# Performance work log

Measured on AMD Instinct MI355X. Metric: run time of the kernel, lower is better.

The kernel has to match this reference:

```python
import jax, jax.numpy as jnp
import numpy as np
from jax import lax

B, C, H, W = 1, 128, 56, 56
NH, NG, KS = 4, 1, 3
CG = C // NG          # channels per group
CH = C // NH          # channels per head
NHG = NH // NG        # heads per group
SCALE = CH ** -0.5


def _norm_grid(h, w, n):
    # matches _get_normalized_grid: (y, x) order, each normalized to [-1, 1]
    y = jnp.arange(h, dtype=jnp.float32) / (h - 1.0) * 2.0 - 1.0
    x = jnp.arange(w, dtype=jnp.float32) / (w - 1.0) * 2.0 - 1.0
    g = jnp.stack(jnp.meshgrid(y, x, indexing='ij'), axis=-1)  # (h, w, 2)
    return jnp.broadcast_to(g[None], (n, h, w, 2))


def _grid_sample(img, grid):
    # F.grid_sample: bilinear, align_corners=True, zeros padding; grid is (x, y) in [-1, 1]
    n, c, hi, wi = img.shape
    gs = grid.shape[1:-1]
    gx = grid[..., 0].reshape(n, -1)
    gy = grid[..., 1].reshape(n, -1)
    fx = (gx + 1.0) * 0.5 * (wi - 1)
    fy = (gy + 1.0) * 0.5 * (hi - 1)
    x0 = jnp.floor(fx)
    y0 = jnp.floor(fy)
    wx = fx - x0
    wy = fy - y0
    x0 = x0.astype(jnp.int32)
    y0 = y0.astype(jnp.int32)
    imgf = img.reshape(n, c, hi * wi)

    def corner(xi, yi, wgt):
        valid = (xi >= 0) & (xi < wi) & (yi >= 0) & (yi < hi)
        idx = jnp.clip(yi, 0, hi - 1) * wi + jnp.clip(xi, 0, wi - 1)
        vals = jax.vmap(lambda im, ii: jnp.take(im, ii, axis=1))(imgf, idx)  # (n, c, P)
        return vals * (wgt * valid)[:, None, :]

    out = (corner(x0, y0, (1 - wx) * (1 - wy)) + corner(x0 + 1, y0, wx * (1 - wy))
           + corner(x0, y0 + 1, (1 - wx) * wy) + corner(x0 + 1, y0 + 1, wx * wy))
    return out.reshape((n, c) + gs)


def _conv1x1(t, w, b):
    return jnp.einsum('bchw,oc->bohw', t, w) + b[None, :, None, None]


def _forward(x, query, dw_w, dw_b, ln_w, ln_b, pw_w, k_w, k_b, v_w, v_b, out_w, out_b, rpe_table):
    # conv_offset: depthwise 3x3 (stride 1, pad 1) -> channel LayerNorm -> GELU -> 1x1 to 2ch (no bias)
    qg = query.reshape(B * NG, CG, H, W)
    t = lax.conv_general_dilated(qg, dw_w, (1, 1), ((1, 1), (1, 1)),
                                 dimension_numbers=('NCHW', 'OIHW', 'NCHW'),
                                 feature_group_count=CG) + dw_b[None, :, None, None]
    mu = t.mean(axis=1, keepdims=True)
    var = ((t - mu) ** 2).mean(axis=1, keepdims=True)
    t = (t - mu) / jnp.sqrt(var + 1e-5) * ln_w[None, :, None, None] + ln_b[None, :, None, None]
    t = jax.nn.gelu(t, approximate=False)
    offset = jnp.einsum('bchw,oc->bohw', t, pw_w)  # (BG, 2, Hk, Wk) in (y, x) order
    Hk, Wk = offset.shape[-2:]
    n_sample = Hk * Wk

    # tanh-scaled offsets (scale_offset_range=True, factor 0.5)
    rng = jnp.array([1.0 / (Hk - 1.0), 1.0 / (Wk - 1.0)], jnp.float32).reshape(1, 2, 1, 1)
    offset = jnp.tanh(offset) * rng * 0.5
    offset = jnp.transpose(offset, (0, 2, 3, 1))  # (BG, Hk, Wk, 2)

    ref = _norm_grid(Hk, Wk, B * NG)
    rwo = offset + ref  # no clamp in the scale_offset_range branch

    # sample K/V features at deformed locations
    xs = _grid_sample(x.reshape(B * NG, CG, H, W), rwo[..., ::-1])  # (BG, CG, Hk, Wk)
    xs = xs.reshape(B, C, 1, n_sample)

    q = query.reshape(B * NH, CH, H * W)
    k = _conv1x1(xs, k_w, k_b).reshape(B * NH, CH, n_sample)
    v = _conv1x1(xs, v_w, v_b).reshape(B * NH, CH, n_sample)

    attn = jnp.einsum('bcm,bcn->bmn', q, k) * SCALE  # (B*NH, HW, n_sample)

    # relative position bias via bilinear lookup of rpe_table at displacements
    rpe = jnp.broadcast_to(rpe_table[None], (B,) + rpe_table.shape).reshape(B * NG, NHG, 2 * H - 1, 2 * W - 1)
    qgrid = _norm_grid(H, W, B * NG)
    disp = (qgrid.reshape(B * NG, H * W, 2)[:, :, None, :]
            - rwo.reshape(B * NG, n_sample, 2)[:, None, :, :]) * 0.5  # (BG, HW, n_sample, 2)
    bias = _grid_sample(rpe, disp[..., ::-1]).reshape(B * NH, H * W, n_sample)

    attn = jax.nn.softmax(attn + bias, axis=2)
    out = jnp.einsum('bmn,bcn->bcm', attn, v).reshape(B, C, H, W)
    return _conv1x1(out, out_w, out_b)


def setup_inputs() -> dict:
    key = jax.random.key(0)
    ks = jax.random.split(key, 8)
    f = lambda k, sh, s=0.02: jax.random.normal(k, sh, jnp.float32) * s
    return {
        'x': jax.random.normal(ks[0], (B, C, H, W), jnp.float32),
        'query': jax.random.normal(ks[1], (B, C, H, W), jnp.float32),
        'dw_w': f(ks[2], (CG, 1, KS, KS)),
        'dw_b': jnp.zeros((CG,), jnp.float32),
        'ln_w': jnp.ones((CG,), jnp.float32),
        'ln_b': jnp.zeros((CG,), jnp.float32),
        'pw_w': f(ks[3], (2, CG)),
        'k_w': f(ks[4], (C, C)),
        'k_b': jnp.zeros((C,), jnp.float32),
        'v_w': f(ks[5], (C, C)),
        'v_b': jnp.zeros((C,), jnp.float32),
        'out_w': f(ks[6], (C, C)),
        'out_b': jnp.zeros((C,), jnp.float32),
        'rpe_table': f(ks[7], (NH, 2 * H - 1, 2 * W - 1), 0.01),
    }


def reference(x, query, dw_w, dw_b, ln_w, ln_b, pw_w, k_w, k_b, v_w, v_b, out_w, out_b, rpe_table):
    return _forward(x, query, dw_w, dw_b, ln_w, ln_b, pw_w, k_w, k_b, v_w, v_b, out_w, out_b, rpe_table)
```

## Files before the change

kernel.cpp:

```cpp
#include <hip/hip_runtime.h>
#include <hip/hip_bf16.h>
#include <math.h>

#define HH 56
#define WW 56
#define HW 3136
#define NHEAD 4
#define RP 111
#define TP 113
#define TPE 12769
#define SCALE 0.17677669529663687f
#define LOG2E 1.44269504088896f
#define QSC (SCALE * LOG2E)
#define CLEN 224
#define BLEN 448
#define NSTEP 7

typedef unsigned short ushortT;
typedef __attribute__((ext_vector_type(8))) short short8v;
typedef __attribute__((ext_vector_type(16))) float f32x16;

#define OFF_AA   8192u
#define OFF_W4   12288u
#define OFF_KBF  24832u
#define OFF_VBF  225536u
#define OFF_QBF  426240u
#define OFF_KWT  1028352u
#define OFF_VWT  1044736u
#define OFF_OWT  1061120u
#define OFF_XT   1077504u
#define OFF_QT   1478912u
#define OFF_TP2  1880320u
#define OFF_ATT2 1982976u
#define OFF_SUM  (OFF_ATT2 + 401408u)
#define ZERO_F4  103504u

__device__ __forceinline__ ushortT f2bf(float f) {
    unsigned u = __float_as_uint(f);
    u += 0x7fffu + ((u >> 16) & 1u);
    return (ushortT)(u >> 16);
}

__device__ __forceinline__ unsigned cvtpk(float lo, float hi) {
    unsigned r;
    asm("v_cvt_pk_bf16_f32 %0, %1, %2" : "=v"(r) : "v"(lo), "v"(hi));
    return r;
}

__device__ __forceinline__ float fexp2(float x) {
    float r;
    asm("v_exp_f32 %0, %1" : "=v"(r) : "v"(x));
    return r;
}

__device__ __forceinline__ float wave_sum(float v) {
#pragma unroll
    for (int o = 1; o < 64; o <<= 1) v += __shfl_xor(v, o);
    return v;
}

__global__ __launch_bounds__(256) void prep_all_kernel(
    const float* __restrict__ kw, const float* __restrict__ vw, const float* __restrict__ ow,
    const float* __restrict__ rpe, const float* __restrict__ x, const float* __restrict__ query,
    float* __restrict__ kwT, float* __restrict__ vwT, float* __restrict__ owT,
    float2* __restrict__ tp2, float* __restrict__ xT, float* __restrict__ qT,
    ushortT* __restrict__ qbf, float* __restrict__ zbase) {
    const int job = blockIdx.y;
    __shared__ float tile[32][33];
    if (job < 3) {
        int i = blockIdx.x * 256 + threadIdx.x;
        if (i >= 16384) return;
        const float* srcw = (job == 0) ? kw : (job == 1) ? vw : ow;
        float* dstw       = (job == 0) ? kwT : (job == 1) ? vwT : owT;
        dstw[(i & 127) * 128 + (i >> 7)] = srcw[i];
    } else if (job == 3) {
        int i = blockIdx.x * 256 + threadIdx.x;
        if (i >= NHEAD * TPE) return;
        int hd = i / TPE, r = i % TPE;
        int py = r / TP, px = r % TP;
        float v0 = 0.f, v1 = 0.f;
        if (py >= 1 && py <= RP) {
            if (px >= 1 && px <= RP) v0 = rpe[hd * RP * RP + (py - 1) * RP + (px - 1)] * LOG2E;
            if (px <= RP - 1)        v1 = rpe[hd * RP * RP + (py - 1) * RP + px] * LOG2E;
        }
        tp2[i] = make_float2(v0, v1);
    } else if (job == 6) {
        int i = blockIdx.x * 256 + threadIdx.x;
        if (i < ZERO_F4) ((float4*)zbase)[i] = make_float4(0.f, 0.f, 0.f, 0.f);
    } else {
        int bx = blockIdx.x;
        if (bx >= 392) return;
        const float* src = (job == 5) ? query : x;
        float* dst       = (job == 5) ? qT : xT;
        int pt = (bx % 98) * 32, ct = (bx / 98) * 32;
        int jj = threadIdx.x & 31, ii = threadIdx.x >> 5;
#pragma unroll
        for (int r = 0; r < 4; r++)
            tile[ii + r * 8][jj] = src[(ct + ii + r * 8) * HW + pt + jj];
        __syncthreads();
#pragma unroll
        for (int r = 0; r < 4; r++) {
            int p = pt + ii + r * 8, cc = ct + jj;
            float val = tile[jj][ii + r * 8];
            dst[p * 128 + cc] = val;
            if (job == 5)
                qbf[(size_t)((cc >> 5) * HW + p) * 32 + (cc & 31)] = f2bf(val * QSC);
        }
    }
}

__global__ __launch_bounds__(128) void sample_kv_kernel(
    const float* __restrict__ xT, const float* __restrict__ qT,
    const float* __restrict__ dww, const float* __restrict__ dwb,
    const float* __restrict__ lnw, const float* __restrict__ lnb,
    const float* __restrict__ pww,
    const float* __restrict__ kwT, const float* __restrict__ vwT,
    const float* __restrict__ kb, const float* __restrict__ vb,
    ushortT* __restrict__ kbf, ushortT* __restrict__ vbf,
    int* __restrict__ aa, float4* __restrict__ w4g) {
    const int n0 = blockIdx.x * 8;
    const int tid = threadIdx.x;
    const int h = n0 / WW, w0 = n0 % WW;
    const int wid = tid >> 6;
    const bool l0 = ((tid & 63) == 0);

    __shared__ float xs[128 * 9];
    __shared__ int   cidx[8][4];
    __shared__ float cw[8][4];
    __shared__ ushortT kst[8][128];
    __shared__ float red_a[2][8], red_b[2][8], red_y[2][8], red_x[2][8];

    float dwwr[9];
#pragma unroll
    for (int k = 0; k < 9; k++) dwwr[k] = dww[tid * 9 + k];
    float qv[3][10];
#pragma unroll
    for (int ky = 0; ky < 3; ky++) {
        int yy = h + ky - 1;
        bool vy = (unsigned)yy < (unsigned)HH;
#pragma unroll
        for (int t = 0; t < 10; t++) {
            int xx = w0 + t - 1;
            bool v = vy && ((unsigned)xx < (unsigned)WW);
            qv[ky][t] = v ? qT[(yy * WW + xx) * 128 + tid] : 0.f;
        }
    }
    float tj[8];
#pragma unroll
    for (int j = 0; j < 8; j++) {
        float t = dwb[tid];
#pragma unroll
        for (int ky = 0; ky < 3; ky++)
#pragma unroll
            for (int kx = 0; kx < 3; kx++)
                t += qv[ky][j + kx] * dwwr[ky * 3 + kx];
        tj[j] = t;
    }
#pragma unroll
    for (int j = 0; j < 8; j++) { float s = wave_sum(tj[j]); if (l0) red_a[wid][j] = s; }
    __syncthreads();
    float dj[8];
#pragma unroll
    for (int j = 0; j < 8; j++) {
        float mu = (red_a[0][j] + red_a[1][j]) * (1.f / 128.f);
        dj[j] = tj[j] - mu;
        float s = wave_sum(dj[j] * dj[j]);
        if (l0) red_b[wid][j] = s;
    }
    __syncthreads();
    float py = pww[tid], px = pww[128 + tid];
#pragma unroll
    for (int j = 0; j < 8; j++) {
        float var = (red_b[0][j] + red_b[1][j]) * (1.f / 128.f);
        float tn = dj[j] / sqrtf(var + 1e-5f) * lnw[tid] + lnb[tid];
        float g = 0.5f * tn * (1.f + erff(tn * 0.70710678118654752f));
        float sy = wave_sum(g * py);
        float sx = wave_sum(g * px);
        if (l0) { red_y[wid][j] = sy; red_x[wid][j] = sx; }
    }
    __syncthreads();

    if (tid < 8) {
        int j = tid;
        float thy = tanhf(red_y[0][j] + red_y[1][j]);
        float thx = tanhf(red_x[0][j] + red_x[1][j]);
        int hh = h, ww2 = w0 + j;
        float gy = thy * (0.5f / 55.f) + ((float)hh * (2.f / 55.f) - 1.f);
        float gx = thx * (0.5f / 55.f) + ((float)ww2 * (2.f / 55.f) - 1.f);
        float fx = (gx + 1.f) * 27.5f;
        float fy = (gy + 1.f) * 27.5f;
        float x0f = floorf(fx), y0f = floorf(fy);
        float wx = fx - x0f, wy = fy - y0f;
        int x0 = (int)x0f, y0 = (int)y0f;
#pragma unroll
        for (int k = 0; k < 4; k++) {
            int xi = x0 + (k & 1), yi = y0 + (k >> 1);
            float wgt = ((k & 1) ? wx : 1.f - wx) * ((k >> 1) ? wy : 1.f - wy);
            bool v = (xi >= 0) && (xi < WW) && (yi >= 0) && (yi < HH);
            cidx[j][k] = min(max(yi, 0), HH - 1) * WW + min(max(xi, 0), WW - 1);
            cw[j][k] = v ? wgt : 0.f;
        }
        float ty = 55.f - (float)hh - 0.25f * thy;
        float tx = 55.f - (float)ww2 - 0.25f * thx;
        float tyf = floorf(ty), txf = floorf(tx);
        float wyb = ty - tyf, wxb = tx - txf;
        aa[n0 + j] = ((int)tyf) * TP + (int)txf + TP + 1;
        float4 wv;
        wv.x = (1.f - wxb) * (1.f - wyb);
        wv.y = wxb * (1.f - wyb);
        wv.z = (1.f - wxb) * wyb;
        wv.w = wxb * wyb;
        w4g[n0 + j] = wv;
    }
    __syncthreads();

#pragma unroll
    for (int j = 0; j < 8; j++) {
        float s = cw[j][0] * xT[cidx[j][0] * 128 + tid]
                + cw[j][1] * xT[cidx[j][1] * 128 + tid]
                + cw[j][2] * xT[cidx[j][2] * 128 + tid]
                + cw[j][3] * xT[cidx[j][3] * 128 + tid];
        xs[tid * 9 + j] = s;
    }
    __syncthreads();

    float ak[8], av[8];
#pragma unroll
    for (int j = 0; j < 8; j++) { ak[j] = 0.f; av[j] = 0.f; }
    for (int c = 0; c < 128; c++) {
        float wk = kwT[c * 128 + tid];
        float wv = vwT[c * 128 + tid];
#pragma unroll
        for (int j = 0; j < 8; j++) {
            float xv = xs[c * 9 + j];
            ak[j] += wk * xv;
            av[j] += wv * xv;
        }
    }
    float kbv = kb[tid], vbv = vb[tid];
    int hh2 = tid >> 5, ch = tid & 31;

    unsigned vp[4];
#pragma unroll
    for (int q = 0; q < 4; q++)
        vp[q] = (unsigned)f2bf(av[2 * q] + vbv) | ((unsigned)f2bf(av[2 * q + 1] + vbv) << 16);
    *(uint4*)(vbf + (size_t)(hh2 * 32 + ch) * HW + n0) = make_uint4(vp[0], vp[1], vp[2], vp[3]);

#pragma unroll
    for (int j = 0; j < 8; j++) kst[j][tid] = f2bf(ak[j] + kbv);
    __syncthreads();
#pragma unroll
    for (int r = 0; r < 4; r++) {
        int lin = tid + 128 * r;
        int j = lin >> 6, dd = lin & 63;
        int o = 2 * dd;
        unsigned val = *(unsigned*)&kst[j][o];
        int hd2 = o >> 5, ch2 = o & 31;
        ((unsigned*)kbf)[((size_t)(hd2 * HW + n0 + j) * 32 + ch2) >> 1] = val;
    }
}

__device__ __forceinline__ void mkw(float pa0, float pa1, float pb0, float pb1, int h,
                                    unsigned &wlo, unsigned &whi) {
    float ta0 = __shfl_xor(pa0, 32);
    float ta1 = __shfl_xor(pa1, 32);
    float tb0 = __shfl_xor(pb0, 32);
    float tb1 = __shfl_xor(pb1, 32);
    wlo = cvtpk(h ? tb0 : pa0, h ? tb1 : pa1);
    whi = cvtpk(h ? pb0 : ta0, h ? pb1 : ta1);
}

__global__ __launch_bounds__(256) void attn_kernel(
    const ushortT* __restrict__ qbf, const ushortT* __restrict__ kbf,
    const ushortT* __restrict__ vbf,
    const int* __restrict__ aa, const float4* __restrict__ w4,
    const float2* __restrict__ tp2g, float* __restrict__ att2, float* __restrict__ sums) {
    const int bx = blockIdx.x;
    const int mtile = blockIdx.y;
    const int hd = blockIdx.z;
    const int tid = threadIdx.x;
    const int wv = tid >> 6;
    const int msub = wv & 1;
    const int csub = wv >> 1;
    const int l = tid & 63;
    const int lm = l & 31;
    const int h = l >> 5;

    const int N0 = bx * BLEN;
    const int m0 = mtile * 64;
    const int mg = m0 + msub * 32 + lm;

    __shared__ int aa_s[BLEN];
    __shared__ float4 w4_s[BLEN];
    __shared__ float2 tpw[12 * TP];

    const int h_min = N0 / WW;
    const int rm0 = m0 / WW, rm1 = (m0 + 63) / WW;
    const int R0 = 48 - h_min + rm0;
    const int NR = 10 + rm1 - rm0;
    const int rbase = R0 * TP;

    const float2* srcw = tp2g + hd * TPE + rbase;
    for (int i = tid; i < NR * TP; i += 256) tpw[i] = srcw[i];
    for (int i = tid; i < BLEN; i += 256) {
        aa_s[i] = aa[N0 + i] - rbase;
        w4_s[i] = w4[N0 + i];
    }
    __syncthreads();

    const int base_m = (mg / WW) * TP + (mg % WW);

    const ushortT* qb = qbf + (size_t)(hd * HW + mg) * 32 + h * 8;
    short8v qf0 = *(const short8v*)(qb);
    short8v qf1 = *(const short8v*)(qb + 16);

    const int nwave = N0 + csub * CLEN;
    const ushortT* kbp = kbf + (size_t)(hd * HW + nwave) * 32;
    const ushortT* vbp = vbf + (size_t)(hd * 32 + lm) * HW + nwave;

    f32x16 accO;
#pragma unroll
    for (int i = 0; i < 16; i++) accO[i] = 0.f;
    float ssum = 0.f;

    for (int nt = 0; nt < NSTEP; ++nt) {
        const ushortT* ka = kbp + (size_t)(nt * 32 + lm) * 32 + h * 8;
        short8v kf0 = *(const short8v*)(ka);
        short8v kf1 = *(const short8v*)(ka + 16);
        f32x16 s;
#pragma unroll
        for (int i = 0; i < 16; i++) s[i] = 0.f;
        s = __builtin_amdgcn_mfma_f32_32x32x16_bf16(kf0, qf0, s, 0, 0, 0);
        s = __builtin_amdgcn_mfma_f32_32x32x16_bf16(kf1, qf1, s, 0, 0, 0);

        float p[16];
#pragma unroll
        for (int r = 0; r < 16; ++r) {
            int nl = csub * CLEN + nt * 32 + (r & 3) + 8 * (r >> 2) + 4 * h;
            int a0 = aa_s[nl] + base_m;
            float4 wvv = w4_s[nl];
            float2 t01 = tpw[a0];
            float2 t23 = tpw[a0 + TP];
            float bias = wvv.x * t01.x + wvv.y * t01.y + wvv.z * t23.x + wvv.w * t23.y;
            float pr = fexp2(s[r] + bias);
            ssum += pr;
            p[r] = pr;
        }

        union { unsigned u[4]; short8v s8; } A0, A1;
        mkw(p[0], p[1], p[4], p[5], h, A0.u[0], A0.u[2]);
        mkw(p[2], p[3], p[6], p[7], h, A0.u[1], A0.u[3]);
        mkw(p[8], p[9], p[12], p[13], h, A1.u[0], A1.u[2]);
        mkw(p[10], p[11], p[14], p[15], h, A1.u[1], A1.u[3]);

        const ushortT* va = vbp + nt * 32 + h * 8;
        short8v vf0 = *(const short8v*)(va);
        short8v vf1 = *(const short8v*)(va + 16);
        accO = __builtin_amdgcn_mfma_f32_32x32x16_bf16(A0.s8, vf0, accO, 0, 0, 0);
        accO = __builtin_amdgcn_mfma_f32_32x32x16_bf16(A1.s8, vf1, accO, 0, 0, 0);
    }

    float* abase = att2 + (size_t)(hd * HW + m0 + msub * 32) * 32 + lm;
#pragma unroll
    for (int r = 0; r < 16; ++r) {
        int mr = (r & 3) + 8 * (r >> 2) + 4 * h;
        atomicAdd(abase + (size_t)mr * 32, accO[r]);
    }
    float st = ssum + __shfl_xor(ssum, 32);
    if (h == 0) atomicAdd(&sums[hd * HW + mg], st);
}

__global__ __launch_bounds__(128) void combine_out_kernel(
    const float* __restrict__ att2, const float* __restrict__ sums,
    const float* __restrict__ owT, const float* __restrict__ ob, float* __restrict__ out) {
    int m0 = blockIdx.x * 8;
    int tid = threadIdx.x;
    int hd = tid >> 5, c = tid & 31;

    __shared__ float at[128 * 9];
    __shared__ float inv_s[4][8];

    if (tid < 32) {
        int hh = tid >> 3, j = tid & 7;
        inv_s[hh][j] = 1.f / sums[hh * HW + m0 + j];
    }
    __syncthreads();

#pragma unroll
    for (int j = 0; j < 8; j++)
        at[tid * 9 + j] = att2[(size_t)(hd * HW + m0 + j) * 32 + c] * inv_s[hd][j];
    __syncthreads();

    float acc[8];
#pragma unroll
    for (int j = 0; j < 8; j++) acc[j] = 0.f;
    for (int cc = 0; cc < 128; cc++) {
        float w = owT[cc * 128 + tid];
        const float* arow = at + cc * 9;
#pragma unroll
        for (int j = 0; j < 8; j++) acc[j] += w * arow[j];
    }
    float b = ob[tid];
#pragma unroll
    for (int j = 0; j < 8; j++) out[tid * HW + m0 + j] = acc[j] + b;
}

extern "C" void kernel_launch(void* const* d_in, const int* in_sizes, int n_in,
                              void* d_out, int out_size, void* d_ws, size_t ws_size,
                              hipStream_t stream) {
    const float* x     = (const float*)d_in[0];
    const float* query = (const float*)d_in[1];
    const float* dww   = (const float*)d_in[2];
    const float* dwb   = (const float*)d_in[3];
    const float* lnw   = (const float*)d_in[4];
    const float* lnb   = (const float*)d_in[5];
    const float* pww   = (const float*)d_in[6];
    const float* kw    = (const float*)d_in[7];
    const float* kb    = (const float*)d_in[8];
    const float* vw    = (const float*)d_in[9];
    const float* vb    = (const float*)d_in[10];
    const float* ow    = (const float*)d_in[11];
    const float* ob    = (const float*)d_in[12];
    const float* rpe   = (const float*)d_in[13];
    float* out = (float*)d_out;
    float* ws  = (float*)d_ws;

    prep_all_kernel<<<dim3(405, 7), 256, 0, stream>>>(
        kw, vw, ow, rpe, x, query,
        ws + OFF_KWT, ws + OFF_VWT, ws + OFF_OWT, (float2*)(ws + OFF_TP2),
        ws + OFF_XT, ws + OFF_QT, (ushortT*)(ws + OFF_QBF), ws + OFF_ATT2);
    sample_kv_kernel<<<392, 128, 0, stream>>>(
        ws + OFF_XT, ws + OFF_QT, dww, dwb, lnw, lnb, pww,
        ws + OFF_KWT, ws + OFF_VWT, kb, vb,
        (ushortT*)(ws + OFF_KBF), (ushortT*)(ws + OFF_VBF),
        (int*)(ws + OFF_AA), (float4*)(ws + OFF_W4));
    attn_kernel<<<dim3(7, 49, NHEAD), 256, 0, stream>>>(
        (const ushortT*)(ws + OFF_QBF), (const ushortT*)(ws + OFF_KBF),
        (const ushortT*)(ws + OFF_VBF),
        (const int*)(ws + OFF_AA), (const float4*)(ws + OFF_W4),
        (const float2*)(ws + OFF_TP2), ws + OFF_ATT2, ws + OFF_SUM);
    combine_out_kernel<<<392, 128, 0, stream>>>(ws + OFF_ATT2, ws + OFF_SUM,
                                                ws + OFF_OWT, ob, out);
}
```

Measured before the change: 161.0 us.

## Pack four bilinear RPE corners per entry and halve attention key slab size

The precomputed RPE table now stores all four bilinear corner values per position as a float4, so the bias gather becomes one LDS read instead of two float2 reads. The attention grid doubles its key-slab count to 14 with 224 keys per block. The two column-half waves now interleave 32-key steps (csub, csub+2, ...) instead of taking contiguous halves. This shrinks the per-block shared RPE window to 6 rows and raises grid parallelism. In exchange the table doubles in size, the two waves get uneven step counts (4 vs 3), and there are twice as many atomic adds to the output accumulators.

```diff
diff --git a/kernel.cpp b/kernel.cpp
--- a/kernel.cpp
+++ b/kernel.cpp
@@ -12,9 +12,8 @@
 #define SCALE 0.17677669529663687f
 #define LOG2E 1.44269504088896f
 #define QSC (SCALE * LOG2E)
-#define CLEN 224
-#define BLEN 448
-#define NSTEP 7
+#define BLEN 224
+#define NSLAB 14
 
 typedef unsigned short ushortT;
 typedef __attribute__((ext_vector_type(8))) short short8v;
@@ -30,8 +29,8 @@
 #define OFF_OWT  1061120u
 #define OFF_XT   1077504u
 #define OFF_QT   1478912u
-#define OFF_TP2  1880320u
-#define OFF_ATT2 1982976u
+#define OFF_TP4  1880320u
+#define OFF_ATT2 2084672u
 #define OFF_SUM  (OFF_ATT2 + 401408u)
 #define ZERO_F4  103504u
 
@@ -63,7 +62,7 @@
     const float* __restrict__ kw, const float* __restrict__ vw, const float* __restrict__ ow,
     const float* __restrict__ rpe, const float* __restrict__ x, const float* __restrict__ query,
     float* __restrict__ kwT, float* __restrict__ vwT, float* __restrict__ owT,
-    float2* __restrict__ tp2, float* __restrict__ xT, float* __restrict__ qT,
+    float4* __restrict__ tp4, float* __restrict__ xT, float* __restrict__ qT,
     ushortT* __restrict__ qbf, float* __restrict__ zbase) {
     const int job = blockIdx.y;
     __shared__ float tile[32][33];
@@ -78,12 +77,17 @@
         if (i >= NHEAD * TPE) return;
         int hd = i / TPE, r = i % TPE;
         int py = r / TP, px = r % TP;
-        float v0 = 0.f, v1 = 0.f;
-        if (py >= 1 && py <= RP) {
-            if (px >= 1 && px <= RP) v0 = rpe[hd * RP * RP + (py - 1) * RP + (px - 1)] * LOG2E;
-            if (px <= RP - 1)        v1 = rpe[hd * RP * RP + (py - 1) * RP + px] * LOG2E;
-        }
-        tp2[i] = make_float2(v0, v1);
+        const float* tb = rpe + hd * RP * RP;
+        bool ry0 = (py >= 1) && (py <= RP);
+        bool ry1 = (py <= RP - 1);
+        bool cx0 = (px >= 1) && (px <= RP);
+        bool cx1 = (px <= RP - 1);
+        float4 v;
+        v.x = (ry0 && cx0) ? tb[(py - 1) * RP + (px - 1)] * LOG2E : 0.f;
+        v.y = (ry0 && cx1) ? tb[(py - 1) * RP + px] * LOG2E : 0.f;
+        v.z = (ry1 && cx0) ? tb[py * RP + (px - 1)] * LOG2E : 0.f;
+        v.w = (ry1 && cx1) ? tb[py * RP + px] * LOG2E : 0.f;
+        tp4[i] = v;
     } else if (job == 6) {
         int i = blockIdx.x * 256 + threadIdx.x;
         if (i < ZERO_F4) ((float4*)zbase)[i] = make_float4(0.f, 0.f, 0.f, 0.f);
@@ -274,7 +278,7 @@
     const ushortT* __restrict__ qbf, const ushortT* __restrict__ kbf,
     const ushortT* __restrict__ vbf,
     const int* __restrict__ aa, const float4* __restrict__ w4,
-    const float2* __restrict__ tp2g, float* __restrict__ att2, float* __restrict__ sums) {
+    const float4* __restrict__ tp4g, float* __restrict__ att2, float* __restrict__ sums) {
     const int bx = blockIdx.x;
     const int mtile = blockIdx.y;
     const int hd = blockIdx.z;
@@ -292,19 +296,18 @@
 
     __shared__ int aa_s[BLEN];
     __shared__ float4 w4_s[BLEN];
-    __shared__ float2 tpw[12 * TP];
-
-    const int h_min = N0 / WW;
-    const int rm0 = m0 / WW, rm1 = (m0 + 63) / WW;
-    const int R0 = 48 - h_min + rm0;
-    const int NR = 10 + rm1 - rm0;
+    __shared__ float4 tpw[6 * TP];
+
+    const int h0 = bx * 4;
+    const int rm0 = m0 / WW;
+    const int R0 = 52 - h0 + rm0;
     const int rbase = R0 * TP;
 
-    const float2* srcw = tp2g + hd * TPE + rbase;
-    for (int i = tid; i < NR * TP; i += 256) tpw[i] = srcw[i];
-    for (int i = tid; i < BLEN; i += 256) {
-        aa_s[i] = aa[N0 + i] - rbase;
-        w4_s[i] = w4[N0 + i];
+    const float4* srcw = tp4g + (size_t)hd * TPE + rbase;
+    for (int i = tid; i < 6 * TP; i += 256) tpw[i] = srcw[i];
+    if (tid < BLEN) {
+        aa_s[tid] = aa[N0 + tid] - rbase;
+        w4_s[tid] = w4[N0 + tid];
     }
     __syncthreads();
 
@@ -314,17 +317,13 @@
     short8v qf0 = *(const short8v*)(qb);
     short8v qf1 = *(const short8v*)(qb + 16);
 
-    const int nwave = N0 + csub * CLEN;
-    const ushortT* kbp = kbf + (size_t)(hd * HW + nwave) * 32;
-    const ushortT* vbp = vbf + (size_t)(hd * 32 + lm) * HW + nwave;
-
     f32x16 accO;
 #pragma unroll
     for (int i = 0; i < 16; i++) accO[i] = 0.f;
     float ssum = 0.f;
 
-    for (int nt = 0; nt < NSTEP; ++nt) {
-        const ushortT* ka = kbp + (size_t)(nt * 32 + lm) * 32 + h * 8;
+    for (int nt = csub; nt < 7; nt += 2) {
+        const ushortT* ka = kbf + (size_t)(hd * HW + N0 + nt * 32 + lm) * 32 + h * 8;
         short8v kf0 = *(const short8v*)(ka);
         short8v kf1 = *(const short8v*)(ka + 16);
         f32x16 s;
@@ -336,12 +335,11 @@
         float p[16];
 #pragma unroll
         for (int r = 0; r < 16; ++r) {
-            int nl = csub * CLEN + nt * 32 + (r & 3) + 8 * (r >> 2) + 4 * h;
+            int nl = nt * 32 + (r & 3) + 8 * (r >> 2) + 4 * h;
             int a0 = aa_s[nl] + base_m;
             float4 wvv = w4_s[nl];
-            float2 t01 = tpw[a0];
-            float2 t23 = tpw[a0 + TP];
-            float bias = wvv.x * t01.x + wvv.y * t01.y + wvv.z * t23.x + wvv.w * t23.y;
+            float4 t4 = tpw[a0];
+            float bias = wvv.x * t4.x + wvv.y * t4.y + wvv.z * t4.z + wvv.w * t4.w;
             float pr = fexp2(s[r] + bias);
             ssum += pr;
             p[r] = pr;
@@ -353,7 +351,7 @@
         mkw(p[8], p[9], p[12], p[13], h, A1.u[0], A1.u[2]);
         mkw(p[10], p[11], p[14], p[15], h, A1.u[1], A1.u[3]);
 
-        const ushortT* va = vbp + nt * 32 + h * 8;
+        const ushortT* va = vbf + (size_t)(hd * 32 + lm) * HW + N0 + nt * 32 + h * 8;
         short8v vf0 = *(const short8v*)(va);
         short8v vf1 = *(const short8v*)(va + 16);
         accO = __builtin_amdgcn_mfma_f32_32x32x16_bf16(A0.s8, vf0, accO, 0, 0, 0);
@@ -427,18 +425,18 @@
 
     prep_all_kernel<<<dim3(405, 7), 256, 0, stream>>>(
         kw, vw, ow, rpe, x, query,
-        ws + OFF_KWT, ws + OFF_VWT, ws + OFF_OWT, (float2*)(ws + OFF_TP2),
+        ws + OFF_KWT, ws + OFF_VWT, ws + OFF_OWT, (float4*)(ws + OFF_TP4),
         ws + OFF_XT, ws + OFF_QT, (ushortT*)(ws + OFF_QBF), ws + OFF_ATT2);
     sample_kv_kernel<<<392, 128, 0, stream>>>(
         ws + OFF_XT, ws + OFF_QT, dww, dwb, lnw, lnb, pww,
         ws + OFF_KWT, ws + OFF_VWT, kb, vb,
         (ushortT*)(ws + OFF_KBF), (ushortT*)(ws + OFF_VBF),
         (int*)(ws + OFF_AA), (float4*)(ws + OFF_W4));
-    attn_kernel<<<dim3(7, 49, NHEAD), 256, 0, stream>>>(
+    attn_kernel<<<dim3(NSLAB, 49, NHEAD), 256, 0, stream>>>(
         (const ushortT*)(ws + OFF_QBF), (const ushortT*)(ws + OFF_KBF),
         (const ushortT*)(ws + OFF_VBF),
         (const int*)(ws + OFF_AA), (const float4*)(ws + OFF_W4),
-        (const float2*)(ws + OFF_TP2), ws + OFF_ATT2, ws + OFF_SUM);
+        (const float4*)(ws + OFF_TP4), ws + OFF_ATT2, ws + OFF_SUM);
     combine_out_kernel<<<392, 128, 0, stream>>>(ws + OFF_ATT2, ws + OFF_SUM,
                                                 ws + OFF_OWT, ob, out);
 }
```

After: 171.5 us. +6.5%, slower.
